# Optimization experiments

Measured on AMD Instinct MI355X. Metric: run time of the kernel, lower is better.

## Reference

```python
import jax, jax.numpy as jnp
import numpy as np

HID = 1024; HEADS = 16; HD = 64; INTER = 4096; NLAYERS = 4
PATCH = 16; IMG_SIZE = 1024; MAXSIDE = IMG_SIZE // PATCH
THETA = 10000.0; EPS = 1e-5; SCALE = HD ** -0.5


def setup_inputs() -> dict:
    key = jax.random.key(0)
    ks = jax.random.split(key, 11)
    s = 0.02
    w = lambda k, shape: jax.random.normal(k, shape, jnp.float32) * s
    return {
        "img0": jax.random.normal(ks[0], (3, 512, 512), jnp.float32),
        "img1": jax.random.normal(ks[1], (3, 512, 256), jnp.float32),
        "conv_w": w(ks[2], (HID, 3, PATCH, PATCH)),
        "ln_pre_w": jnp.ones((HID,), jnp.float32),
        "attn_norm_w": jnp.ones((NLAYERS, HID), jnp.float32),
        "q_w": w(ks[3], (NLAYERS, HID, HID)),
        "k_w": w(ks[4], (NLAYERS, HID, HID)),
        "v_w": w(ks[5], (NLAYERS, HID, HID)),
        "o_w": w(ks[6], (NLAYERS, HID, HID)),
        "ffn_norm_w": jnp.ones((NLAYERS, HID), jnp.float32),
        "gate_w": w(ks[7], (NLAYERS, INTER, HID)),
        "up_w": w(ks[8], (NLAYERS, INTER, HID)),
        "down_w": w(ks[9], (NLAYERS, HID, INTER)),
    }


def _rms(x, wt):
    return x * jax.lax.rsqrt(jnp.mean(x * x, axis=-1, keepdims=True) + EPS) * wt


def _rot_half(x):
    return jnp.concatenate([-x[..., HD // 2:], x[..., :HD // 2]], axis=-1)


def reference(img0, img1, conv_w, ln_pre_w, attn_norm_w, q_w, k_w, v_w, o_w,
              ffn_norm_w, gate_w, up_w, down_w):
    dn = ('NCHW', 'OIHW', 'NCHW')
    grids, embeds = [], []
    for img in (img0, img1):
        p = jax.lax.conv_general_dilated(img[None], conv_w, (PATCH, PATCH),
                                         'VALID', dimension_numbers=dn)  # [1,HID,h,w]
        h, wd = p.shape[2], p.shape[3]
        grids.append((h, wd))
        embeds.append(p.reshape(1, HID, h * wd).transpose(0, 2, 1))
    x = jnp.concatenate(embeds, axis=1)  # [1, S, HID]
    S = x.shape[1]
    x = _rms(x, ln_pre_w)

    # meshgrid position ids: h*MAXSIDE + w per image
    pids = jnp.concatenate([
        (jnp.arange(h)[:, None] * MAXSIDE + jnp.arange(wd)[None, :]).reshape(-1)
        for h, wd in grids])
    # Pixtral 2D RoPE frequency table
    freqs = 1.0 / THETA ** (jnp.arange(0, HD, 2, dtype=jnp.float32) / HD)  # [HD/2]
    fh = jnp.outer(jnp.arange(MAXSIDE, dtype=jnp.float32), freqs[::2])   # [64, HD/4]
    fw = jnp.outer(jnp.arange(MAXSIDE, dtype=jnp.float32), freqs[1::2])  # [64, HD/4]
    inv = jnp.concatenate([
        jnp.broadcast_to(fh[:, None, :], (MAXSIDE, MAXSIDE, HD // 4)),
        jnp.broadcast_to(fw[None, :, :], (MAXSIDE, MAXSIDE, HD // 4))],
        axis=-1).reshape(-1, HD // 2)
    inv = jnp.concatenate([inv, inv], axis=-1)  # [MAXSIDE^2, HD]
    emb = inv[pids]                              # [S, HD]
    cos = jnp.cos(emb)[None, None]               # [1,1,S,HD]
    sin = jnp.sin(emb)[None, None]

    # block-diagonal additive mask (images don't attend across each other)
    neg = jnp.finfo(jnp.float32).min
    mask = jnp.full((S, S), neg, jnp.float32)
    off = 0
    for h, wd in grids:
        n = h * wd
        mask = mask.at[off:off + n, off:off + n].set(0.0)
        off += n

    def layer(xc, p):
        an, qw, kw, vw, ow, fn, gw, uw, dw = p
        hn = _rms(xc, an)
        heads = lambda y, wm: jnp.einsum('bsd,ed->bse', y, wm).reshape(
            1, S, HEADS, HD).transpose(0, 2, 1, 3)  # [1,H,S,D]
        q, k, v = heads(hn, qw), heads(hn, kw), heads(hn, vw)
        q = q * cos + _rot_half(q) * sin
        k = k * cos + _rot_half(k) * sin
        scores = jnp.einsum('bhqd,bhkd->bhqk', q, k) * SCALE + mask
        aw = jax.nn.softmax(scores.astype(jnp.float32), axis=-1).astype(xc.dtype)
        o = jnp.einsum('bhqk,bhkd->bhqd', aw, v).transpose(0, 2, 1, 3).reshape(1, S, HID)
        h2 = xc + jnp.einsum('bsd,ed->bse', o, ow)
        m = _rms(h2, fn)
        ff = jnp.einsum(
            'bsi,di->bsd',
            jax.nn.silu(jnp.einsum('bsd,id->bsi', m, gw)) * jnp.einsum('bsd,id->bsi', m, uw),
            dw)
        return h2 + ff, None

    out, _ = jax.lax.scan(layer, x, (attn_norm_w, q_w, k_w, v_w, o_w,
                                     ffn_norm_w, gate_w, up_w, down_w))
    return out
```

## Files before the change

kernel.cpp:

```cpp
#include <hip/hip_runtime.h>
#include <hip/hip_bf16.h>
#include <math.h>

#define S_TOT 1536
#define S0    1024
#define HID   1024
#define HEADS 16
#define HD    64
#define INTER 4096
#define NLAYERS 4
#define KCONV 768
#define EPSV  1e-5f
#define SCALEV 0.125f
#define QKS   2048

typedef __attribute__((ext_vector_type(8))) __bf16 bf16x8;
typedef __attribute__((ext_vector_type(8))) unsigned short u16x8;
typedef __attribute__((ext_vector_type(4))) float f32x4;
typedef __attribute__((address_space(1))) void gvoid;
typedef __attribute__((address_space(3))) void lvoid;

__device__ __forceinline__ ushort f2bf(float f) {
    union { float f; unsigned u; } v; v.f = f;
    unsigned u = v.u;
    return (ushort)((u + 0x7FFFu + ((u >> 16) & 1u)) >> 16);
}
__device__ __forceinline__ float bf2f(ushort b) {
    union { unsigned u; float f; } v; v.u = ((unsigned)b) << 16;
    return v.f;
}

template<int N> __device__ __forceinline__ void wait_vm() {
    if constexpr (N == 0)      asm volatile("s_waitcnt vmcnt(0)" ::: "memory");
    else if constexpr (N == 2) asm volatile("s_waitcnt vmcnt(2)" ::: "memory");
    else if constexpr (N == 4) asm volatile("s_waitcnt vmcnt(4)" ::: "memory");
    else if constexpr (N == 8) asm volatile("s_waitcnt vmcnt(8)" ::: "memory");
    else                       asm volatile("s_waitcnt vmcnt(0)" ::: "memory");
}

__global__ __launch_bounds__(256) void cvt_kernel(
    const float* __restrict__ src, ushort* __restrict__ dst, int n4)
{
    int i = blockIdx.x * 256 + threadIdx.x;
    if (i < n4) {
        float4 v = ((const float4*)src)[i];
        ushort4 o;
        o.x = f2bf(v.x); o.y = f2bf(v.y); o.z = f2bf(v.z); o.w = f2bf(v.w);
        ((ushort4*)dst)[i] = o;
    }
}

__global__ __launch_bounds__(256) void cvt_layer_kernel(
    const float* __restrict__ qw, const float* __restrict__ kw,
    const float* __restrict__ vw, const float* __restrict__ ow,
    const float* __restrict__ gw, const float* __restrict__ uw,
    const float* __restrict__ dw, ushort* __restrict__ dst)
{
    int i = blockIdx.x * 256 + threadIdx.x;
    int e = i << 2;
    const float* src; int off; size_t de;
    if      (e < (1  << 20)) { src = qw; off = e;             de = e; }
    else if (e < (2  << 20)) { src = kw; off = e - (1 << 20); de = e; }
    else if (e < (3  << 20)) { src = vw; off = e - (2 << 20); de = e; }
    else if (e < (4  << 20)) { src = ow; off = e - (3 << 20); de = e; }
    else if (e < (8  << 20)) {
        src = gw; off = e - (4 << 20);
        int chan = off >> 10, col = off & 1023;
        de = (size_t)(4 << 20) + (size_t)(((chan >> 4) << 5) + (chan & 15)) * 1024 + col;
    }
    else if (e < (12 << 20)) {
        src = uw; off = e - (8 << 20);
        int chan = off >> 10, col = off & 1023;
        de = (size_t)(4 << 20) + (size_t)(((chan >> 4) << 5) + 16 + (chan & 15)) * 1024 + col;
    }
    else                     { src = dw; off = e - (12 << 20); de = e; }
    float4 v = *(const float4*)(src + off);
    ushort4 o;
    o.x = f2bf(v.x); o.y = f2bf(v.y); o.z = f2bf(v.z); o.w = f2bf(v.w);
    *(ushort4*)(dst + de) = o;
}

__global__ __launch_bounds__(256) void im2col_kernel(
    const float* __restrict__ img0, const float* __restrict__ img1,
    ushort* __restrict__ P)
{
    int s = blockIdx.x;
    const float* img; int W, ph, pw;
    if (s < S0) { img = img0; W = 512; ph = s >> 5; pw = s & 31; }
    else { int t = s - S0; img = img1; W = 256; ph = t >> 4; pw = t & 15; }
    for (int k = threadIdx.x; k < KCONV; k += 256) {
        int c = k >> 8; int r = k & 255; int y = r >> 4; int x = r & 15;
        P[(size_t)s * KCONV + k] =
            f2bf(img[(size_t)c * 512 * W + (size_t)(ph * 16 + y) * W + (pw * 16 + x)]);
    }
}

#define GEMM2P_CORE(BM_, BN_, NLA_, NLB_)                                        \
    auto stage = [&](int b, int k0) {                                            \
        _Pragma("unroll")                                                        \
        for (int i_ = 0; i_ < NLA_; ++i_) {                                      \
            int idx = t + i_ * 256;                                              \
            int r_ = idx >> 2, c8_ = (idx & 3) << 3;                             \
            __builtin_amdgcn_global_load_lds(                                    \
                (gvoid*)(A + (size_t)(bm + r_) * K + k0 + c8_),                  \
                (lvoid*)(&As[b][idx * 8]), 16, 0, 0);                            \
        }                                                                        \
        _Pragma("unroll")                                                        \
        for (int i_ = 0; i_ < NLB_; ++i_) {                                      \
            int idx = t + i_ * 256;                                              \
            int r_ = idx >> 2, c8_ = (idx & 3) << 3;                             \
            __builtin_amdgcn_global_load_lds(                                    \
                (gvoid*)(B + (size_t)(bn + r_) * K + k0 + c8_),                  \
                (lvoid*)(&Bs[b][idx * 8]), 16, 0, 0);                            \
        }                                                                        \
    };

template<int BM, int BN, bool OUT_BF16>
__global__ __launch_bounds__(256) void gemm2p(
    const ushort* __restrict__ A, const ushort* __restrict__ B,
    void* __restrict__ Cout, int M, int N, int K)
{
    constexpr int WMT = BM / 32, WNT = BN / 32;
    constexpr int NLA = (BM * 32) / (8 * 256);
    constexpr int NLB = (BN * 32) / (8 * 256);
    constexpr int NL  = NLA + NLB;
    __shared__ ushort As[2][BM * 32];
    __shared__ ushort Bs[2][BN * 32];
    const int t = threadIdx.x;
    const int bm = blockIdx.x * BM, bn = blockIdx.y * BN;
    const int wave = t >> 6, lane = t & 63;
    const int wm = (wave & 1) * (BM / 2), wn = (wave >> 1) * (BN / 2);
    const int frow = lane & 15, fq = lane >> 4;
    GEMM2P_CORE(BM, BN, NLA, NLB)

    f32x4 acc[WMT][WNT];
    #pragma unroll
    for (int i = 0; i < WMT; ++i)
        #pragma unroll
        for (int j = 0; j < WNT; ++j) acc[i][j] = (f32x4){0.f, 0.f, 0.f, 0.f};

    stage(0, 0);
    int cur = 0;
    for (int k0 = 0; k0 < K; k0 += 32) {
        const bool more = (k0 + 32) < K;
        if (more) { stage(cur ^ 1, k0 + 32); wait_vm<NL>(); }
        else      { wait_vm<0>(); }
        __builtin_amdgcn_s_barrier();
        __builtin_amdgcn_sched_barrier(0);
        bf16x8 af[WMT], bfr[WNT];
        #pragma unroll
        for (int i = 0; i < WMT; ++i)
            af[i] = *(const bf16x8*)(&As[cur][(wm + 16 * i + frow) * 32 + fq * 8]);
        #pragma unroll
        for (int j = 0; j < WNT; ++j)
            bfr[j] = *(const bf16x8*)(&Bs[cur][(wn + 16 * j + frow) * 32 + fq * 8]);
        asm volatile("s_waitcnt lgkmcnt(0)" ::: "memory");
        __builtin_amdgcn_sched_barrier(0);
        __builtin_amdgcn_s_barrier();
        #pragma unroll
        for (int i = 0; i < WMT; ++i)
            #pragma unroll
            for (int j = 0; j < WNT; ++j)
                acc[i][j] = __builtin_amdgcn_mfma_f32_16x16x32_bf16(
                    af[i], bfr[j], acc[i][j], 0, 0, 0);
        cur ^= 1;
    }
    #pragma unroll
    for (int i = 0; i < WMT; ++i) {
        #pragma unroll
        for (int j = 0; j < WNT; ++j) {
            #pragma unroll
            for (int r = 0; r < 4; ++r) {
                int row = bm + wm + 16 * i + fq * 4 + r;
                int col = bn + wn + 16 * j + frow;
                float vv = acc[i][j][r];
                if (OUT_BF16) ((ushort*)Cout)[(size_t)row * N + col] = f2bf(vv);
                else          ((float*)Cout)[(size_t)row * N + col] = vv;
            }
        }
    }
}

__global__ __launch_bounds__(256) void gemm2p_qkv(
    const ushort* __restrict__ A, const ushort* __restrict__ B,
    ushort* __restrict__ qkb, ushort* __restrict__ vb,
    const float* __restrict__ cs, const float* __restrict__ sn, int K)
{
    constexpr int BM = 128, BN = 128;
    __shared__ ushort As[2][BM * 32];
    __shared__ ushort Bs[2][BN * 32];
    const int t = threadIdx.x;
    const int bm = blockIdx.x * BM, bn = blockIdx.y * BN;
    const int wave = t >> 6, lane = t & 63;
    const int wm = (wave & 1) * 64, wn = (wave >> 1) * 64;
    const int frow = lane & 15, fq = lane >> 4;
    GEMM2P_CORE(BM, BN, 2, 2)

    f32x4 acc[4][4];
    #pragma unroll
    for (int i = 0; i < 4; ++i)
        #pragma unroll
        for (int j = 0; j < 4; ++j) acc[i][j] = (f32x4){0.f, 0.f, 0.f, 0.f};

    stage(0, 0);
    int cur = 0;
    for (int k0 = 0; k0 < K; k0 += 32) {
        const bool more = (k0 + 32) < K;
        if (more) { stage(cur ^ 1, k0 + 32); wait_vm<4>(); }
        else      { wait_vm<0>(); }
        __builtin_amdgcn_s_barrier();
        __builtin_amdgcn_sched_barrier(0);
        bf16x8 af[4], bfr[4];
        #pragma unroll
        for (int i = 0; i < 4; ++i)
            af[i] = *(const bf16x8*)(&As[cur][(wm + 16 * i + frow) * 32 + fq * 8]);
        #pragma unroll
        for (int j = 0; j < 4; ++j)
            bfr[j] = *(const bf16x8*)(&Bs[cur][(wn + 16 * j + frow) * 32 + fq * 8]);
        asm volatile("s_waitcnt lgkmcnt(0)" ::: "memory");
        __builtin_amdgcn_sched_barrier(0);
        __builtin_amdgcn_s_barrier();
        #pragma unroll
        for (int i = 0; i < 4; ++i)
            #pragma unroll
            for (int j = 0; j < 4; ++j)
                acc[i][j] = __builtin_amdgcn_mfma_f32_16x16x32_bf16(
                    af[i], bfr[j], acc[i][j], 0, 0, 0);
        cur ^= 1;
    }
    const int colbase = bn + wn;
    const int part = colbase >> 10;
    if (part < 2) {
        #pragma unroll
        for (int i = 0; i < 4; ++i) {
            #pragma unroll
            for (int r = 0; r < 4; ++r) {
                int row = bm + wm + 16 * i + fq * 4 + r;
                float cv0 = cs[row * 32 + frow],      sv0 = sn[row * 32 + frow];
                float cv1 = cs[row * 32 + 16 + frow], sv1 = sn[row * 32 + 16 + frow];
                float xa0 = acc[i][0][r], xa1 = acc[i][1][r];
                float xb0 = acc[i][2][r], xb1 = acc[i][3][r];
                ushort* dst = qkb + (size_t)row * QKS + (part << 10) + (colbase & 1023) + frow;
                dst[0]  = f2bf(xa0 * cv0 - xb0 * sv0);
                dst[16] = f2bf(xa1 * cv1 - xb1 * sv1);
                dst[32] = f2bf(xb0 * cv0 + xa0 * sv0);
                dst[48] = f2bf(xb1 * cv1 + xa1 * sv1);
            }
        }
    } else {
        #pragma unroll
        for (int i = 0; i < 4; ++i)
            #pragma unroll
            for (int j = 0; j < 4; ++j)
                #pragma unroll
                for (int r = 0; r < 4; ++r) {
                    int row = bm + wm + 16 * i + fq * 4 + r;
                    vb[(size_t)row * 1024 + (colbase & 1023) + 16 * j + frow] =
                        f2bf(acc[i][j][r]);
                }
    }
}

__global__ __launch_bounds__(256) void gemm2p_gu(
    const ushort* __restrict__ A, const ushort* __restrict__ B,
    ushort* __restrict__ gb, int K)
{
    constexpr int BM = 128, BN = 128;
    __shared__ ushort As[2][BM * 32];
    __shared__ ushort Bs[2][BN * 32];
    const int t = threadIdx.x;
    const int bm = blockIdx.x * BM, bn = blockIdx.y * BN;
    const int wave = t >> 6, lane = t & 63;
    const int wm = (wave & 1) * 64, wn = (wave >> 1) * 64;
    const int frow = lane & 15, fq = lane >> 4;
    GEMM2P_CORE(BM, BN, 2, 2)

    f32x4 acc[4][4];
    #pragma unroll
    for (int i = 0; i < 4; ++i)
        #pragma unroll
        for (int j = 0; j < 4; ++j) acc[i][j] = (f32x4){0.f, 0.f, 0.f, 0.f};

    stage(0, 0);
    int cur = 0;
    for (int k0 = 0; k0 < K; k0 += 32) {
        const bool more = (k0 + 32) < K;
        if (more) { stage(cur ^ 1, k0 + 32); wait_vm<4>(); }
        else      { wait_vm<0>(); }
        __builtin_amdgcn_s_barrier();
        __builtin_amdgcn_sched_barrier(0);
        bf16x8 af[4], bfr[4];
        #pragma unroll
        for (int i = 0; i < 4; ++i)
            af[i] = *(const bf16x8*)(&As[cur][(wm + 16 * i + frow) * 32 + fq * 8]);
        #pragma unroll
        for (int j = 0; j < 4; ++j)
            bfr[j] = *(const bf16x8*)(&Bs[cur][(wn + 16 * j + frow) * 32 + fq * 8]);
        asm volatile("s_waitcnt lgkmcnt(0)" ::: "memory");
        __builtin_amdgcn_sched_barrier(0);
        __builtin_amdgcn_s_barrier();
        #pragma unroll
        for (int i = 0; i < 4; ++i)
            #pragma unroll
            for (int j = 0; j < 4; ++j)
                acc[i][j] = __builtin_amdgcn_mfma_f32_16x16x32_bf16(
                    af[i], bfr[j], acc[i][j], 0, 0, 0);
        cur ^= 1;
    }
    #pragma unroll
    for (int i = 0; i < 4; ++i) {
        #pragma unroll
        for (int jp = 0; jp < 2; ++jp) {
            int chan = ((bn + wn) >> 1) + jp * 16 + frow;
            #pragma unroll
            for (int r = 0; r < 4; ++r) {
                int row = bm + wm + 16 * i + fq * 4 + r;
                float g = acc[i][2 * jp][r], u = acc[i][2 * jp + 1][r];
                float sg = 1.f / (1.f + __expf(-g));
                gb[(size_t)row * INTER + chan] = f2bf(g * sg * u);
            }
        }
    }
}

template<int SPLITK>
__global__ __launch_bounds__(256) void gemm2p_sk(
    const ushort* __restrict__ A, const ushort* __restrict__ B,
    float* __restrict__ P, int M, int N, int K)
{
    constexpr int BM = 128, BN = 128;
    __shared__ ushort As[2][BM * 32];
    __shared__ ushort Bs[2][BN * 32];
    const int t = threadIdx.x;
    const int bm = blockIdx.x * BM, bn = blockIdx.y * BN;
    const int kc = K / SPLITK;
    const int kb = blockIdx.z * kc, ke = kb + kc;
    const int wave = t >> 6, lane = t & 63;
    const int wm = (wave & 1) * 64, wn = (wave >> 1) * 64;
    const int frow = lane & 15, fq = lane >> 4;
    GEMM2P_CORE(BM, BN, 2, 2)

    f32x4 acc[4][4];
    #pragma unroll
    for (int i = 0; i < 4; ++i)
        #pragma unroll
        for (int j = 0; j < 4; ++j) acc[i][j] = (f32x4){0.f, 0.f, 0.f, 0.f};

    stage(0, kb);
    int cur = 0;
    for (int k0 = kb; k0 < ke; k0 += 32) {
        const bool more = (k0 + 32) < ke;
        if (more) { stage(cur ^ 1, k0 + 32); wait_vm<4>(); }
        else      { wait_vm<0>(); }
        __builtin_amdgcn_s_barrier();
        __builtin_amdgcn_sched_barrier(0);
        bf16x8 af[4], bfr[4];
        #pragma unroll
        for (int i = 0; i < 4; ++i)
            af[i] = *(const bf16x8*)(&As[cur][(wm + 16 * i + frow) * 32 + fq * 8]);
        #pragma unroll
        for (int j = 0; j < 4; ++j)
            bfr[j] = *(const bf16x8*)(&Bs[cur][(wn + 16 * j + frow) * 32 + fq * 8]);
        asm volatile("s_waitcnt lgkmcnt(0)" ::: "memory");
        __builtin_amdgcn_sched_barrier(0);
        __builtin_amdgcn_s_barrier();
        #pragma unroll
        for (int i = 0; i < 4; ++i)
            #pragma unroll
            for (int j = 0; j < 4; ++j)
                acc[i][j] = __builtin_amdgcn_mfma_f32_16x16x32_bf16(
                    af[i], bfr[j], acc[i][j], 0, 0, 0);
        cur ^= 1;
    }
    float* Pz = P + (size_t)blockIdx.z * M * N;
    #pragma unroll
    for (int i = 0; i < 4; ++i) {
        #pragma unroll
        for (int j = 0; j < 4; ++j) {
            #pragma unroll
            for (int r = 0; r < 4; ++r) {
                int row = bm + wm + 16 * i + fq * 4 + r;
                int col = bn + wn + 16 * j + frow;
                Pz[(size_t)row * N + col] = acc[i][j][r];
            }
        }
    }
}

__global__ __launch_bounds__(256) void reduce4_kernel(
    const float* __restrict__ P, float* __restrict__ x, int n4)
{
    int i = blockIdx.x * 256 + threadIdx.x;
    if (i >= n4) return;
    const int n = n4 << 2;
    float4 a  = ((const float4*)x)[i];
    float4 p0 = ((const float4*)P)[i];
    float4 p1 = ((const float4*)(P + (size_t)n))[i];
    float4 p2 = ((const float4*)(P + (size_t)2 * n))[i];
    float4 p3 = ((const float4*)(P + (size_t)3 * n))[i];
    a.x += p0.x + p1.x + p2.x + p3.x;
    a.y += p0.y + p1.y + p2.y + p3.y;
    a.z += p0.z + p1.z + p2.z + p3.z;
    a.w += p0.w + p1.w + p2.w + p3.w;
    ((float4*)x)[i] = a;
}

__global__ __launch_bounds__(256) void rms_kernel(
    const float* __restrict__ in, const float* __restrict__ w,
    float* __restrict__ out)
{
    int row = blockIdx.x;
    const float* xr = in + (size_t)row * HID;
    float ss = 0.f;
    for (int i = threadIdx.x; i < HID; i += 256) { float v = xr[i]; ss += v * v; }
    #pragma unroll
    for (int off = 32; off > 0; off >>= 1) ss += __shfl_down(ss, off, 64);
    __shared__ float red[4];
    int wid = threadIdx.x >> 6;
    if ((threadIdx.x & 63) == 0) red[wid] = ss;
    __syncthreads();
    if (threadIdx.x == 0)
        red[0] = rsqrtf((red[0] + red[1] + red[2] + red[3]) / HID + EPSV);
    __syncthreads();
    float rs = red[0];
    for (int i = threadIdx.x; i < HID; i += 256)
        out[(size_t)row * HID + i] = xr[i] * rs * w[i];
}

__global__ __launch_bounds__(256) void rms_bf_kernel(
    const float* __restrict__ in, const float* __restrict__ w,
    ushort* __restrict__ out)
{
    int row = blockIdx.x;
    const float* xr = in + (size_t)row * HID;
    float ss = 0.f;
    for (int i = threadIdx.x; i < HID; i += 256) { float v = xr[i]; ss += v * v; }
    #pragma unroll
    for (int off = 32; off > 0; off >>= 1) ss += __shfl_down(ss, off, 64);
    __shared__ float red[4];
    int wid = threadIdx.x >> 6;
    if ((threadIdx.x & 63) == 0) red[wid] = ss;
    __syncthreads();
    if (threadIdx.x == 0)
        red[0] = rsqrtf((red[0] + red[1] + red[2] + red[3]) / HID + EPSV);
    __syncthreads();
    float rs = red[0];
    for (int i = threadIdx.x; i < HID; i += 256)
        out[(size_t)row * HID + i] = f2bf(xr[i] * rs * w[i]);
}

__global__ void rope_tab_kernel(float* __restrict__ cs, float* __restrict__ sn)
{
    int s = blockIdx.x; int j = threadIdx.x;
    int h, w;
    if (s < S0) { h = s >> 5; w = s & 31; }
    else { int t = s - S0; h = t >> 4; w = t & 15; }
    float f;
    if (j < 16) f = (float)h * powf(10000.f, -(4.f * j) / 64.f);
    else        f = (float)w * powf(10000.f, -(4.f * (j - 16) + 2.f) / 64.f);
    cs[s * 32 + j] = cosf(f);
    sn[s * 32 + j] = sinf(f);
}

__global__ __launch_bounds__(256) void vtrans_bf_kernel(
    const ushort* __restrict__ vb, ushort* __restrict__ vT)
{
    __shared__ ushort T[64][72];
    int st = blockIdx.x;
    int hh = blockIdx.y;
    int s0 = st << 6;
    int t = threadIdx.x;
    #pragma unroll
    for (int i = 0; i < 2; ++i) {
        int u = t + (i << 8);
        int r = u >> 3, c8 = (u & 7) << 3;
        u16x8 v = *(const u16x8*)(vb + (size_t)(s0 + r) * 1024 + hh * HD + c8);
        *(u16x8*)(&T[r][c8]) = v;
    }
    __syncthreads();
    int d = t >> 2, sg = (t & 3) << 4;
    ushort buf[16];
    #pragma unroll
    for (int j = 0; j < 16; ++j) buf[j] = T[sg + j][d];
    ushort* dst = vT + ((size_t)hh * HD + d) * S_TOT + s0 + sg;
    *(u16x8*)dst = *(u16x8*)buf;
    *(u16x8*)(dst + 8) = *(u16x8*)(buf + 8);
}

__global__ __launch_bounds__(256) void flash_mfma_kernel(
    const ushort* __restrict__ qkb, const ushort* __restrict__ vT,
    ushort* __restrict__ o)
{
    __shared__ ushort Ks[64 * 72];
    __shared__ ushort Vt[64 * 72];
    __shared__ ushort Ps[4 * 16 * 72];
    int tile = blockIdx.x;
    int hh = blockIdx.y;
    int segStart, q0, nkt;
    if (tile < 16) { segStart = 0; q0 = tile << 6; nkt = 16; }
    else { segStart = S0; q0 = S0 + ((tile - 16) << 6); nkt = 8; }
    const int t = threadIdx.x;
    const int wave = t >> 6, lane = t & 63;
    const int c = lane & 15, fq = lane >> 4;
    const int wq = wave << 4;
    ushort* Pw = Ps + wave * 16 * 72;

    bf16x8 qf[2];
    #pragma unroll
    for (int ks = 0; ks < 2; ++ks)
        qf[ks] = *(const bf16x8*)(qkb + (size_t)(q0 + wq + c) * QKS + hh * HD + ks * 32 + fq * 8);

    float m_i[4], l_i[4];
    f32x4 accO[4];
    #pragma unroll
    for (int r = 0; r < 4; ++r) { m_i[r] = -1e30f; l_i[r] = 0.f; }
    #pragma unroll
    for (int nt = 0; nt < 4; ++nt) accO[nt] = (f32x4){0.f, 0.f, 0.f, 0.f};

    for (int kt = 0; kt < nkt; ++kt) {
        int kbase = segStart + (kt << 6);
        __syncthreads();
        #pragma unroll
        for (int i = 0; i < 2; ++i) {
            int u = t + (i << 8);
            int r = u >> 3, c8 = (u & 7) << 3;
            u16x8 kv = *(const u16x8*)(qkb + (size_t)(kbase + r) * QKS + 1024 + hh * HD + c8);
            *(u16x8*)(Ks + r * 72 + c8) = kv;
            u16x8 vv = *(const u16x8*)(vT + ((size_t)hh * HD + r) * S_TOT + kbase + c8);
            *(u16x8*)(Vt + r * 72 + c8) = vv;
        }
        __syncthreads();

        f32x4 acc[4];
        #pragma unroll
        for (int nt = 0; nt < 4; ++nt) acc[nt] = (f32x4){0.f, 0.f, 0.f, 0.f};
        #pragma unroll
        for (int ks = 0; ks < 2; ++ks) {
            #pragma unroll
            for (int nt = 0; nt < 4; ++nt) {
                bf16x8 bfr = *(const bf16x8*)(Ks + (nt * 16 + c) * 72 + ks * 32 + fq * 8);
                acc[nt] = __builtin_amdgcn_mfma_f32_16x16x32_bf16(qf[ks], bfr, acc[nt], 0, 0, 0);
            }
        }

        #pragma unroll
        for (int r = 0; r < 4; ++r) {
            float s0v = acc[0][r] * SCALEV, s1v = acc[1][r] * SCALEV;
            float s2v = acc[2][r] * SCALEV, s3v = acc[3][r] * SCALEV;
            float rm = fmaxf(fmaxf(s0v, s1v), fmaxf(s2v, s3v));
            #pragma unroll
            for (int msk = 1; msk < 16; msk <<= 1)
                rm = fmaxf(rm, __shfl_xor(rm, msk, 64));
            float mn = fmaxf(m_i[r], rm);
            float al = __expf(m_i[r] - mn);
            float p0 = __expf(s0v - mn), p1 = __expf(s1v - mn);
            float p2 = __expf(s2v - mn), p3 = __expf(s3v - mn);
            float rs = p0 + p1 + p2 + p3;
            #pragma unroll
            for (int msk = 1; msk < 16; msk <<= 1)
                rs += __shfl_xor(rs, msk, 64);
            l_i[r] = l_i[r] * al + rs;
            m_i[r] = mn;
            #pragma unroll
            for (int nt = 0; nt < 4; ++nt) accO[nt][r] *= al;
            int qrow = (fq << 2) + r;
            Pw[qrow * 72 + 0  + c] = f2bf(p0);
            Pw[qrow * 72 + 16 + c] = f2bf(p1);
            Pw[qrow * 72 + 32 + c] = f2bf(p2);
            Pw[qrow * 72 + 48 + c] = f2bf(p3);
        }

        #pragma unroll
        for (int ks = 0; ks < 2; ++ks) {
            bf16x8 pa = *(const bf16x8*)(Pw + c * 72 + ks * 32 + fq * 8);
            #pragma unroll
            for (int nt = 0; nt < 4; ++nt) {
                bf16x8 bv = *(const bf16x8*)(Vt + (nt * 16 + c) * 72 + ks * 32 + fq * 8);
                accO[nt] = __builtin_amdgcn_mfma_f32_16x16x32_bf16(pa, bv, accO[nt], 0, 0, 0);
            }
        }
    }

    #pragma unroll
    for (int r = 0; r < 4; ++r) {
        float inv = 1.f / l_i[r];
        int row = q0 + wq + (fq << 2) + r;
        #pragma unroll
        for (int nt = 0; nt < 4; ++nt)
            o[(size_t)row * HID + hh * HD + nt * 16 + c] = f2bf(accO[nt][r] * inv);
    }
}

__global__ __launch_bounds__(256) void copy_kernel(
    const float* __restrict__ src, float* __restrict__ dst, int n)
{
    int i = blockIdx.x * 256 + threadIdx.x;
    if (i < n) dst[i] = src[i];
}

extern "C" void kernel_launch(void* const* d_in, const int* in_sizes, int n_in,
                              void* d_out, int out_size, void* d_ws, size_t ws_size,
                              hipStream_t stream)
{
    const float* img0        = (const float*)d_in[0];
    const float* img1        = (const float*)d_in[1];
    const float* conv_w      = (const float*)d_in[2];
    const float* ln_pre_w    = (const float*)d_in[3];
    const float* attn_norm_w = (const float*)d_in[4];
    const float* q_w         = (const float*)d_in[5];
    const float* k_w         = (const float*)d_in[6];
    const float* v_w         = (const float*)d_in[7];
    const float* o_w         = (const float*)d_in[8];
    const float* ffn_norm_w  = (const float*)d_in[9];
    const float* gate_w      = (const float*)d_in[10];
    const float* up_w        = (const float*)d_in[11];
    const float* down_w      = (const float*)d_in[12];

    char* p = (char*)d_ws;
    float* x    = (float*)p;   p += (size_t)1572864 * 4;
    float* cs   = (float*)p;   p += (size_t)49152 * 4;
    float* sn   = (float*)p;   p += (size_t)49152 * 4;
    ushort* qkb = (ushort*)p;  p += (size_t)3145728 * 2;
    ushort* vb  = (ushort*)p;  p += (size_t)1572864 * 2;
    ushort* vTb = (ushort*)p;  p += (size_t)1572864 * 2;
    ushort* hnb = (ushort*)p;  p += (size_t)1572864 * 2;
    ushort* obb = (ushort*)p;  p += (size_t)1572864 * 2;
    ushort* gb  = (ushort*)p;  p += (size_t)6291456 * 2;
    float* skP  = (float*)p;   p += (size_t)6291456 * 4;
    ushort* Pb  = (ushort*)p;  p += (size_t)1179648 * 2;
    ushort* cvb = (ushort*)p;  p += (size_t)786432 * 2;
    ushort* wbuf= (ushort*)p;  p += (size_t)16777216 * 2;

    ushort* wqkv = wbuf;
    ushort* wo   = wbuf + 3145728;
    ushort* wgu  = wbuf + 4194304;
    ushort* wdn  = wbuf + 12582912;

    dim3 blk(256);

    cvt_kernel<<<768, blk, 0, stream>>>(conv_w, cvb, 786432 / 4);
    im2col_kernel<<<S_TOT, blk, 0, stream>>>(img0, img1, Pb);
    gemm2p<64, 64, false><<<dim3(24, 16), blk, 0, stream>>>(
        Pb, cvb, x, S_TOT, HID, KCONV);
    rms_kernel<<<S_TOT, blk, 0, stream>>>(x, ln_pre_w, x);
    rope_tab_kernel<<<S_TOT, 32, 0, stream>>>(cs, sn);

    for (int l = 0; l < NLAYERS; ++l) {
        cvt_layer_kernel<<<16384, blk, 0, stream>>>(
            q_w + (size_t)l * 1048576, k_w + (size_t)l * 1048576,
            v_w + (size_t)l * 1048576, o_w + (size_t)l * 1048576,
            gate_w + (size_t)l * 4194304, up_w + (size_t)l * 4194304,
            down_w + (size_t)l * 4194304, wbuf);

        rms_bf_kernel<<<S_TOT, blk, 0, stream>>>(x, attn_norm_w + (size_t)l * HID, hnb);
        gemm2p_qkv<<<dim3(12, 24), blk, 0, stream>>>(
            hnb, wqkv, qkb, vb, cs, sn, HID);
        vtrans_bf_kernel<<<dim3(24, HEADS), blk, 0, stream>>>(vb, vTb);
        flash_mfma_kernel<<<dim3(24, HEADS), blk, 0, stream>>>(qkb, vTb, obb);
        gemm2p_sk<4><<<dim3(12, 8, 4), blk, 0, stream>>>(
            obb, wo, skP, S_TOT, HID, HID);
        reduce4_kernel<<<1536, blk, 0, stream>>>(skP, x, S_TOT * HID / 4);
        rms_bf_kernel<<<S_TOT, blk, 0, stream>>>(x, ffn_norm_w + (size_t)l * HID, hnb);
        gemm2p_gu<<<dim3(12, 64), blk, 0, stream>>>(hnb, wgu, gb, HID);
        gemm2p_sk<4><<<dim3(12, 8, 4), blk, 0, stream>>>(
            gb, wdn, skP, S_TOT, HID, INTER);
        reduce4_kernel<<<1536, blk, 0, stream>>>(skP, x, S_TOT * HID / 4);
    }
    copy_kernel<<<(S_TOT * HID) / 256, blk, 0, stream>>>(x, (float*)d_out, S_TOT * HID);
}
```

Before: 927.9 us.

## Use 256x256 triple-buffered gate/up GEMM and fuse split-K reduce with RMSNorm

The gate/up GEMM moves from 128x128 tiles with 256 threads and double buffering to 256x256 tiles with 512 threads. It adds triple-buffered LDS staging, XOR-swizzled LDS layout, an XCD-aware block remap, and raised priority around the MFMA loop. Separately, the split-K reduction after the O projection is fused with the following RMSNorm-to-bf16 kernel, which saves one launch and one pass over the residual. Larger tiles cut redundant global loads, but they use far more LDS (96KB) and registers, and leave only 192 blocks, which may underfill the GPU.

```diff
diff --git a/kernel.cpp b/kernel.cpp
--- a/kernel.cpp
+++ b/kernel.cpp
@@ -261,61 +261,86 @@
     }
 }
 
-__global__ __launch_bounds__(256) void gemm2p_gu(
+__global__ __launch_bounds__(512, 2) void gemm_gu8(
     const ushort* __restrict__ A, const ushort* __restrict__ B,
     ushort* __restrict__ gb, int K)
 {
-    constexpr int BM = 128, BN = 128;
-    __shared__ ushort As[2][BM * 32];
-    __shared__ ushort Bs[2][BN * 32];
+    __shared__ ushort As[3][256 * 32];
+    __shared__ ushort Bs[3][256 * 32];
     const int t = threadIdx.x;
-    const int bm = blockIdx.x * BM, bn = blockIdx.y * BN;
+    int wg = blockIdx.x + gridDim.x * blockIdx.y;
+    int q = (gridDim.x * gridDim.y) >> 3;
+    int wgs = (wg & 7) * q + (wg >> 3);
+    const int bm = (wgs % gridDim.x) * 256;
+    const int bn = (wgs / gridDim.x) * 256;
     const int wave = t >> 6, lane = t & 63;
-    const int wm = (wave & 1) * 64, wn = (wave >> 1) * 64;
+    const int wm = (wave >> 2) * 128, wn = (wave & 3) * 64;
     const int frow = lane & 15, fq = lane >> 4;
-    GEMM2P_CORE(BM, BN, 2, 2)
-
-    f32x4 acc[4][4];
-    #pragma unroll
-    for (int i = 0; i < 4; ++i)
+
+    auto stage = [&](int b, int k0) {
+        #pragma unroll
+        for (int i = 0; i < 2; ++i) {
+            int sl = t + (i << 9);
+            int r = sl >> 2, sp = sl & 3;
+            int lc = sp ^ (r & 3);
+            __builtin_amdgcn_global_load_lds(
+                (gvoid*)(A + (size_t)(bm + r) * K + k0 + (lc << 3)),
+                (lvoid*)(&As[b][sl * 8]), 16, 0, 0);
+            __builtin_amdgcn_global_load_lds(
+                (gvoid*)(B + (size_t)(bn + r) * K + k0 + (lc << 3)),
+                (lvoid*)(&Bs[b][sl * 8]), 16, 0, 0);
+        }
+    };
+
+    f32x4 acc[8][4];
+    #pragma unroll
+    for (int i = 0; i < 8; ++i)
         #pragma unroll
         for (int j = 0; j < 4; ++j) acc[i][j] = (f32x4){0.f, 0.f, 0.f, 0.f};
 
-    stage(0, 0);
-    int cur = 0;
-    for (int k0 = 0; k0 < K; k0 += 32) {
-        const bool more = (k0 + 32) < K;
-        if (more) { stage(cur ^ 1, k0 + 32); wait_vm<4>(); }
-        else      { wait_vm<0>(); }
+    const int NKT = K >> 5;
+    stage(0, 0); stage(1, 32);
+    int cbuf = 0, sbuf = 2;
+    for (int kt = 0; kt < NKT; ++kt) {
+        if (kt + 1 < NKT) wait_vm<4>();
+        else              wait_vm<0>();
+        __builtin_amdgcn_sched_barrier(0);
         __builtin_amdgcn_s_barrier();
         __builtin_amdgcn_sched_barrier(0);
-        bf16x8 af[4], bfr[4];
-        #pragma unroll
-        for (int i = 0; i < 4; ++i)
-            af[i] = *(const bf16x8*)(&As[cur][(wm + 16 * i + frow) * 32 + fq * 8]);
-        #pragma unroll
-        for (int j = 0; j < 4; ++j)
-            bfr[j] = *(const bf16x8*)(&Bs[cur][(wn + 16 * j + frow) * 32 + fq * 8]);
-        asm volatile("s_waitcnt lgkmcnt(0)" ::: "memory");
-        __builtin_amdgcn_sched_barrier(0);
-        __builtin_amdgcn_s_barrier();
-        #pragma unroll
-        for (int i = 0; i < 4; ++i)
+        if (kt + 2 < NKT) {
+            stage(sbuf, (kt + 2) << 5);
+            sbuf = (sbuf == 2) ? 0 : sbuf + 1;
+        }
+        bf16x8 af[8], bfr[4];
+        #pragma unroll
+        for (int i = 0; i < 8; ++i) {
+            int ar = wm + (i << 4) + frow;
+            af[i] = *(const bf16x8*)(&As[cbuf][(ar << 5) + ((fq ^ (ar & 3)) << 3)]);
+        }
+        #pragma unroll
+        for (int j = 0; j < 4; ++j) {
+            int br = wn + (j << 4) + frow;
+            bfr[j] = *(const bf16x8*)(&Bs[cbuf][(br << 5) + ((fq ^ (br & 3)) << 3)]);
+        }
+        __builtin_amdgcn_s_setprio(1);
+        #pragma unroll
+        for (int i = 0; i < 8; ++i)
             #pragma unroll
             for (int j = 0; j < 4; ++j)
                 acc[i][j] = __builtin_amdgcn_mfma_f32_16x16x32_bf16(
                     af[i], bfr[j], acc[i][j], 0, 0, 0);
-        cur ^= 1;
-    }
-    #pragma unroll
-    for (int i = 0; i < 4; ++i) {
-        #pragma unroll
-        for (int jp = 0; jp < 2; ++jp) {
-            int chan = ((bn + wn) >> 1) + jp * 16 + frow;
+        __builtin_amdgcn_s_setprio(0);
+        cbuf = (cbuf == 2) ? 0 : cbuf + 1;
+    }
+    #pragma unroll
+    for (int i = 0; i < 8; ++i) {
+        #pragma unroll
+        for (int p = 0; p < 2; ++p) {
+            int chan = ((bn + wn) >> 1) + p * 16 + frow;
             #pragma unroll
             for (int r = 0; r < 4; ++r) {
-                int row = bm + wm + 16 * i + fq * 4 + r;
-                float g = acc[i][2 * jp][r], u = acc[i][2 * jp + 1][r];
+                int row = bm + wm + (i << 4) + (fq << 2) + r;
+                float g = acc[i][2 * p][r], u = acc[i][2 * p + 1][r];
                 float sg = 1.f / (1.f + __expf(-g));
                 gb[(size_t)row * INTER + chan] = f2bf(g * sg * u);
             }
@@ -403,6 +428,37 @@
     a.z += p0.z + p1.z + p2.z + p3.z;
     a.w += p0.w + p1.w + p2.w + p3.w;
     ((float4*)x)[i] = a;
+}
+
+__global__ __launch_bounds__(256) void reduce_rms_bf_kernel(
+    const float* __restrict__ P, float* __restrict__ x,
+    const float* __restrict__ w, ushort* __restrict__ out)
+{
+    int row = blockIdx.x, t = threadIdx.x;
+    size_t off = (size_t)row * HID + t * 4;
+    float4 a = *(const float4*)(x + off);
+    #pragma unroll
+    for (int z = 0; z < 4; ++z) {
+        float4 p = *(const float4*)(P + (size_t)z * S_TOT * HID + off);
+        a.x += p.x; a.y += p.y; a.z += p.z; a.w += p.w;
+    }
+    *(float4*)(x + off) = a;
+    float ss = a.x * a.x + a.y * a.y + a.z * a.z + a.w * a.w;
+    #pragma unroll
+    for (int o = 32; o > 0; o >>= 1) ss += __shfl_down(ss, o, 64);
+    __shared__ float red[4];
+    int wid = t >> 6;
+    if ((t & 63) == 0) red[wid] = ss;
+    __syncthreads();
+    if (t == 0)
+        red[0] = rsqrtf((red[0] + red[1] + red[2] + red[3]) / HID + EPSV);
+    __syncthreads();
+    float rs = red[0];
+    const float* wp = w + t * 4;
+    ushort4 o4;
+    o4.x = f2bf(a.x * rs * wp[0]); o4.y = f2bf(a.y * rs * wp[1]);
+    o4.z = f2bf(a.z * rs * wp[2]); o4.w = f2bf(a.w * rs * wp[3]);
+    *(ushort4*)(out + off) = o4;
 }
 
 __global__ __launch_bounds__(256) void rms_kernel(
@@ -659,9 +715,9 @@
         flash_mfma_kernel<<<dim3(24, HEADS), blk, 0, stream>>>(qkb, vTb, obb);
         gemm2p_sk<4><<<dim3(12, 8, 4), blk, 0, stream>>>(
             obb, wo, skP, S_TOT, HID, HID);
-        reduce4_kernel<<<1536, blk, 0, stream>>>(skP, x, S_TOT * HID / 4);
-        rms_bf_kernel<<<S_TOT, blk, 0, stream>>>(x, ffn_norm_w + (size_t)l * HID, hnb);
-        gemm2p_gu<<<dim3(12, 64), blk, 0, stream>>>(hnb, wgu, gb, HID);
+        reduce_rms_bf_kernel<<<S_TOT, blk, 0, stream>>>(
+            skP, x, ffn_norm_w + (size_t)l * HID, hnb);
+        gemm_gu8<<<dim3(6, 32), dim3(512), 0, stream>>>(hnb, wgu, gb, HID);
         gemm2p_sk<4><<<dim3(12, 8, 4), blk, 0, stream>>>(
             gb, wdn, skP, S_TOT, HID, INTER);
         reduce4_kernel<<<1536, blk, 0, stream>>>(skP, x, S_TOT * HID / 4);
```

Result: slower. 959.6 us (+3.4%).
